# Kernel optimization log

Measured on AMD Instinct MI355X. Metric: run time of the kernel, lower is better.

The kernel has to match this reference:

```python
import jax, jax.numpy as jnp
import numpy as np

EPSILON = 1e-8
DT = 0.1
STEPS = 3
MASK_DENSITY = 0.01


def setup_inputs() -> dict:
    key = jax.random.key(0)
    k1, k2 = jax.random.split(key)
    B, S, D = 4, 4096, 2
    psi = jax.random.normal(k1, (B, S, D), dtype=jnp.float32)
    # binary mask: threshold a uniform draw to get a sparse 0/1 adjacency
    u = jax.random.uniform(k2, (B, S, S), dtype=jnp.float32)
    binary_mask = (u < MASK_DENSITY).astype(jnp.float32)
    return {"psi": psi, "binary_mask": binary_mask}


def reference(psi, binary_mask):
    def force(state):
        # adjacency-weighted aggregation minus self: [B,S,S] @ [B,S,2]
        return jnp.einsum('bij,bjd->bid', binary_mask, state) - state

    def step(p, _):
        r = jnp.linalg.norm(p, axis=-1, keepdims=True)          # [B,S,1]
        k1 = force(p)
        psi_star = p + DT * k1
        star_norm = jnp.linalg.norm(psi_star, axis=-1, keepdims=True)
        psi_star = psi_star * (r / (star_norm + EPSILON))       # renormalize to r
        k2 = force(psi_star)
        p_new = p + 0.5 * DT * (k1 + k2)
        new_norm = jnp.linalg.norm(p_new, axis=-1, keepdims=True)
        p_new = p_new * (r / (new_norm + EPSILON))              # norm-preserving
        return p_new, None

    psi_out, _ = jax.lax.scan(step, psi, None, length=STEPS)
    return psi_out
```

## Files before the change

### kernel.cpp

```cpp
#include <hip/hip_runtime.h>
#include <stdint.h>

#define BATCH   4
#define SEQ     4096
#define NROWS   (BATCH * SEQ)
#define SLOTS   80
#define SENT    SEQ
#define PSTR    4224
#define DTS     0.1f
#define HALF_DT 0.05f
#define EPS     1e-8f

typedef float fx4 __attribute__((ext_vector_type(4)));

__device__ __forceinline__ float2 ballot_force_sum(unsigned long long w,
                                                   const float2* __restrict__ gb,
                                                   int lane) {
    const int colbase = ((lane >> 2) << 8) | (lane & 3);
    float sx = 0.f, sy = 0.f;
    while (w) {
        int j = __builtin_ctzll(w);
        w &= (w - 1);
        float2 v = gb[colbase + (j << 2)];
        sx += v.x; sy += v.y;
    }
#pragma unroll
    for (int m = 32; m >= 1; m >>= 1) {
        sx += __shfl_xor(sx, m, 64);
        sy += __shfl_xor(sy, m, 64);
    }
    return make_float2(sx, sy);
}

__global__ __launch_bounds__(256)
void compress_phaseA(const float* __restrict__ mask,
                     const float2* __restrict__ psi,
                     ushort* __restrict__ idx,
                     float2* __restrict__ k1buf,
                     float2* __restrict__ star,
                     float2* __restrict__ pbuf,
                     float*  __restrict__ rbuf) {
    const int row  = (blockIdx.x * blockDim.x + threadIdx.x) >> 6;
    const int lane = threadIdx.x & 63;

    const fx4* src = reinterpret_cast<const fx4*>(mask + (size_t)row * SEQ);
    unsigned long long word = 0ull;
#pragma unroll
    for (int c = 0; c < 16; ++c) {
        fx4 v = __builtin_nontemporal_load(&src[c * 64 + lane]);
        unsigned long long b;
        b = __ballot(v.x != 0.f); if (lane == c * 4 + 0) word = b;
        b = __ballot(v.y != 0.f); if (lane == c * 4 + 1) word = b;
        b = __ballot(v.z != 0.f); if (lane == c * 4 + 2) word = b;
        b = __ballot(v.w != 0.f); if (lane == c * 4 + 3) word = b;
    }

    int pc  = __popcll(word);
    int inc = pc;
#pragma unroll
    for (int ofs = 1; ofs < 64; ofs <<= 1) {
        int t = __shfl_up(inc, ofs, 64);
        if (lane >= ofs) inc += t;
    }
    int pos   = inc - pc;
    int total = __shfl(inc, 63, 64);

    ushort* dst = idx + (size_t)row * SLOTS;
    const int colbase = ((lane >> 2) << 8) | (lane & 3);
    unsigned long long w = word;
    while (w) {
        int j = __builtin_ctzll(w);
        w &= (w - 1);
        if (pos < SLOTS) dst[pos] = (ushort)(colbase + (j << 2));
        ++pos;
    }
    for (int s = total + lane; s < SLOTS; s += 64) dst[s] = (ushort)SENT;

    const int bidx = row >> 12;
    const int rloc = row & 4095;
    float2 sum = ballot_force_sum(word, psi + ((size_t)bidx << 12), lane);
    float2 p  = psi[row];
    float r   = sqrtf(p.x * p.x + p.y * p.y);
    float k1x = sum.x - p.x, k1y = sum.y - p.y;
    float tx  = p.x + DTS * k1x, ty = p.y + DTS * k1y;
    float sc  = r / (sqrtf(tx * tx + ty * ty) + EPS);
    if (lane == 0) {
        k1buf[row] = make_float2(k1x, k1y);
        rbuf[row]  = r;
        star[(size_t)bidx * PSTR + rloc] = make_float2(tx * sc, ty * sc);
        if (rloc == 0) {
            star[(size_t)bidx * PSTR + SENT] = make_float2(0.f, 0.f);
            pbuf[(size_t)bidx * PSTR + SENT] = make_float2(0.f, 0.f);
        }
    }
}

template <int PHASE>
__global__ __launch_bounds__(256)
void force_step(const ushort* __restrict__ idx,
                const float2* __restrict__ pIn, int pinStr,
                const float2* __restrict__ gath,
                float2* __restrict__ k1buf,
                float*  __restrict__ rbuf,
                float2* __restrict__ outbuf, int outStr) {
    __shared__ float2 lds[SEQ + 2];
    const int tid  = blockIdx.x * blockDim.x + threadIdx.x;
    const int row  = tid >> 4;
    const int q    = tid & 15;
    const int bidx = row >> 12;
    const int rloc = row & 4095;
    const float2* __restrict__ gb = gath + (size_t)bidx * PSTR;

    {
        const float4* __restrict__ g4 = reinterpret_cast<const float4*>(gb);
        float4* l4 = reinterpret_cast<float4*>(lds);
#pragma unroll
        for (int t = 0; t < 8; ++t)
            l4[threadIdx.x + t * 256] = g4[threadIdx.x + t * 256];
        if (threadIdx.x == 0) lds[SENT] = gb[SENT];
    }

    const ushort* __restrict__ ip = idx + (size_t)row * SLOTS;
    int c[5];
#pragma unroll
    for (int r = 0; r < 5; ++r) c[r] = ip[q * 5 + r];
    float2 pg = make_float2(0.f, 0.f), k1 = make_float2(0.f, 0.f);
    float  rv = 0.f;
    if (PHASE == 1) {
        pg = pIn[(size_t)bidx * pinStr + rloc];
        k1 = k1buf[row];
        rv = rbuf[row];
    }

    __syncthreads();

    float sx = 0.f, sy = 0.f;
#pragma unroll
    for (int r = 0; r < 5; ++r) {
        float2 v = lds[c[r]];
        sx += v.x; sy += v.y;
    }
#pragma unroll
    for (int m = 8; m >= 1; m >>= 1) {
        sx += __shfl_xor(sx, m, 64);
        sy += __shfl_xor(sy, m, 64);
    }

    if (q == 0) {
        if (PHASE == 0) {
            float2 p  = lds[rloc];
            float r   = sqrtf(p.x * p.x + p.y * p.y);
            float k1x = sx - p.x, k1y = sy - p.y;
            float tx  = p.x + DTS * k1x, ty = p.y + DTS * k1y;
            float sc  = r / (sqrtf(tx * tx + ty * ty) + EPS);
            k1buf[row] = make_float2(k1x, k1y);
            rbuf[row]  = r;
            outbuf[(size_t)bidx * outStr + rloc] = make_float2(tx * sc, ty * sc);
        } else {
            float2 st = lds[rloc];
            float k2x = sx - st.x, k2y = sy - st.y;
            float nx  = pg.x + HALF_DT * (k1.x + k2x);
            float ny  = pg.y + HALF_DT * (k1.y + k2y);
            float sc  = rv / (sqrtf(nx * nx + ny * ny) + EPS);
            outbuf[(size_t)bidx * outStr + rloc] = make_float2(nx * sc, ny * sc);
        }
    }
}

extern "C" void kernel_launch(void* const* d_in, const int* in_sizes, int n_in,
                              void* d_out, int out_size, void* d_ws, size_t ws_size,
                              hipStream_t stream) {
    const float* psi  = (const float*)d_in[0];
    const float* mask = (const float*)d_in[1];
    float2* out2 = (float2*)d_out;

    char* ws = (char*)d_ws;
    ushort* idx = (ushort*)ws;
    float2* pbuf = (float2*)(ws + (size_t)NROWS * SLOTS * sizeof(ushort));
    float2* star = pbuf + (size_t)BATCH * PSTR;
    float2* k1   = star + (size_t)BATCH * PSTR;
    float*  rbuf = (float*)(k1 + NROWS);

    const float2* psi2 = (const float2*)psi;

    compress_phaseA<<<NROWS / 4, 256, 0, stream>>>(mask, psi2, idx, k1, star, pbuf, rbuf);
    force_step<1><<<NROWS / 16, 256, 0, stream>>>(idx, psi2, SEQ, star, k1, rbuf, pbuf, PSTR);
    force_step<0><<<NROWS / 16, 256, 0, stream>>>(idx, pbuf, PSTR, pbuf, k1, rbuf, star, PSTR);
    force_step<1><<<NROWS / 16, 256, 0, stream>>>(idx, pbuf, PSTR, star, k1, rbuf, pbuf, PSTR);
    force_step<0><<<NROWS / 16, 256, 0, stream>>>(idx, pbuf, PSTR, pbuf, k1, rbuf, star, PSTR);
    force_step<1><<<NROWS / 16, 256, 0, stream>>>(idx, pbuf, PSTR, star, k1, rbuf, out2, SEQ);
}
```

Measured before the change: 355.5 us.

## Fuse five force-step launches into one persistent kernel with grid barriers

Replaces the five separate force_step launches with a single persistent kernel of 256 blocks of 1024 threads, separated by a software grid-wide atomic barrier. The goal is to remove per-launch overhead and kernel drain/fill gaps between the small force phases. Each block now reloads its batch's source vector into LDS every phase, and the sentinel slot is zeroed in LDS instead of global memory. It relies on all 256 blocks being co-resident, risks deadlock if they are not, and adds spin-wait and memset costs.

```diff
diff --git a/kernel.cpp b/kernel.cpp
--- a/kernel.cpp
+++ b/kernel.cpp
@@ -6,10 +6,12 @@
 #define NROWS   (BATCH * SEQ)
 #define SLOTS   80
 #define SENT    SEQ
-#define PSTR    4224
 #define DTS     0.1f
 #define HALF_DT 0.05f
 #define EPS     1e-8f
+
+#define NBLK    256
+#define NTHR    1024
 
 typedef float fx4 __attribute__((ext_vector_type(4)));
 
@@ -37,8 +39,7 @@
                      const float2* __restrict__ psi,
                      ushort* __restrict__ idx,
                      float2* __restrict__ k1buf,
-                     float2* __restrict__ star,
-                     float2* __restrict__ pbuf,
+                     float2* __restrict__ starbuf,
                      float*  __restrict__ rbuf) {
     const int row  = (blockIdx.x * blockDim.x + threadIdx.x) >> 6;
     const int lane = threadIdx.x & 63;
@@ -77,7 +78,6 @@
     for (int s = total + lane; s < SLOTS; s += 64) dst[s] = (ushort)SENT;
 
     const int bidx = row >> 12;
-    const int rloc = row & 4095;
     float2 sum = ballot_force_sum(word, psi + ((size_t)bidx << 12), lane);
     float2 p  = psi[row];
     float r   = sqrtf(p.x * p.x + p.y * p.y);
@@ -85,85 +85,105 @@
     float tx  = p.x + DTS * k1x, ty = p.y + DTS * k1y;
     float sc  = r / (sqrtf(tx * tx + ty * ty) + EPS);
     if (lane == 0) {
-        k1buf[row] = make_float2(k1x, k1y);
-        rbuf[row]  = r;
-        star[(size_t)bidx * PSTR + rloc] = make_float2(tx * sc, ty * sc);
-        if (rloc == 0) {
-            star[(size_t)bidx * PSTR + SENT] = make_float2(0.f, 0.f);
-            pbuf[(size_t)bidx * PSTR + SENT] = make_float2(0.f, 0.f);
-        }
-    }
-}
-
-template <int PHASE>
-__global__ __launch_bounds__(256)
-void force_step(const ushort* __restrict__ idx,
-                const float2* __restrict__ pIn, int pinStr,
-                const float2* __restrict__ gath,
-                float2* __restrict__ k1buf,
-                float*  __restrict__ rbuf,
-                float2* __restrict__ outbuf, int outStr) {
-    __shared__ float2 lds[SEQ + 2];
-    const int tid  = blockIdx.x * blockDim.x + threadIdx.x;
-    const int row  = tid >> 4;
-    const int q    = tid & 15;
+        k1buf[row]   = make_float2(k1x, k1y);
+        rbuf[row]    = r;
+        starbuf[row] = make_float2(tx * sc, ty * sc);
+    }
+}
+
+__device__ __forceinline__ void gbar(int* __restrict__ bar, int gen) {
+    __syncthreads();
+    if (threadIdx.x == 0) {
+        __threadfence();
+        atomicAdd(bar, 1);
+        while (__hip_atomic_load(bar, __ATOMIC_RELAXED,
+                                 __HIP_MEMORY_SCOPE_AGENT) < gen * NBLK)
+            __builtin_amdgcn_s_sleep(2);
+        __threadfence();
+    }
+    __syncthreads();
+}
+
+__global__ __launch_bounds__(NTHR)
+void forces(const ushort* __restrict__ idx,
+            const float2* __restrict__ psi,
+            float2* __restrict__ pbuf,
+            float2* __restrict__ star,
+            float2* __restrict__ k1buf,
+            float*  __restrict__ rbuf,
+            float2* __restrict__ out,
+            int*    __restrict__ bar) {
+    __shared__ float2 SRC[SEQ + 2];
+
+    const int t    = threadIdx.x;
+    const int g    = t >> 4;
+    const int q    = t & 15;
+    const int row  = (blockIdx.x << 6) + g;
     const int bidx = row >> 12;
     const int rloc = row & 4095;
-    const float2* __restrict__ gb = gath + (size_t)bidx * PSTR;
-
-    {
-        const float4* __restrict__ g4 = reinterpret_cast<const float4*>(gb);
-        float4* l4 = reinterpret_cast<float4*>(lds);
-#pragma unroll
-        for (int t = 0; t < 8; ++t)
-            l4[threadIdx.x + t * 256] = g4[threadIdx.x + t * 256];
-        if (threadIdx.x == 0) lds[SENT] = gb[SENT];
-    }
+    const size_t bo = (size_t)bidx << 12;
 
     const ushort* __restrict__ ip = idx + (size_t)row * SLOTS;
     int c[5];
 #pragma unroll
     for (int r = 0; r < 5; ++r) c[r] = ip[q * 5 + r];
-    float2 pg = make_float2(0.f, 0.f), k1 = make_float2(0.f, 0.f);
-    float  rv = 0.f;
-    if (PHASE == 1) {
-        pg = pIn[(size_t)bidx * pinStr + rloc];
-        k1 = k1buf[row];
-        rv = rbuf[row];
-    }
-
-    __syncthreads();
-
-    float sx = 0.f, sy = 0.f;
-#pragma unroll
-    for (int r = 0; r < 5; ++r) {
-        float2 v = lds[c[r]];
-        sx += v.x; sy += v.y;
-    }
-#pragma unroll
-    for (int m = 8; m >= 1; m >>= 1) {
-        sx += __shfl_xor(sx, m, 64);
-        sy += __shfl_xor(sy, m, 64);
-    }
-
-    if (q == 0) {
-        if (PHASE == 0) {
-            float2 p  = lds[rloc];
-            float r   = sqrtf(p.x * p.x + p.y * p.y);
-            float k1x = sx - p.x, k1y = sy - p.y;
-            float tx  = p.x + DTS * k1x, ty = p.y + DTS * k1y;
-            float sc  = r / (sqrtf(tx * tx + ty * ty) + EPS);
-            k1buf[row] = make_float2(k1x, k1y);
-            rbuf[row]  = r;
-            outbuf[(size_t)bidx * outStr + rloc] = make_float2(tx * sc, ty * sc);
-        } else {
-            float2 st = lds[rloc];
-            float k2x = sx - st.x, k2y = sy - st.y;
-            float nx  = pg.x + HALF_DT * (k1.x + k2x);
-            float ny  = pg.y + HALF_DT * (k1.y + k2y);
-            float sc  = rv / (sqrtf(nx * nx + ny * ny) + EPS);
-            outbuf[(size_t)bidx * outStr + rloc] = make_float2(nx * sc, ny * sc);
-        }
+
+    int gen = 0;
+#pragma unroll 1
+    for (int ph = 0; ph < 5; ++ph) {
+        const bool isA = (ph & 1);
+        const float2* __restrict__ gb = (isA ? pbuf : star) + bo;
+
+        {
+            const float4* __restrict__ s4 = reinterpret_cast<const float4*>(gb);
+            float4* l4 = reinterpret_cast<float4*>(SRC);
+            l4[t] = s4[t];
+            l4[t + 1024] = s4[t + 1024];
+            if (t == 0) SRC[SEQ] = make_float2(0.f, 0.f);
+        }
+        float2 p = make_float2(0.f, 0.f), k1 = make_float2(0.f, 0.f);
+        float  rv = 0.f;
+        if (!isA) {
+            p  = (ph == 0) ? psi[row] : pbuf[row];
+            k1 = k1buf[row];
+            rv = rbuf[row];
+        }
+        __syncthreads();
+
+        float sx = 0.f, sy = 0.f;
+#pragma unroll
+        for (int r = 0; r < 5; ++r) {
+            float2 v = SRC[c[r]];
+            sx += v.x; sy += v.y;
+        }
+#pragma unroll
+        for (int m = 8; m >= 1; m >>= 1) {
+            sx += __shfl_xor(sx, m, 64);
+            sy += __shfl_xor(sy, m, 64);
+        }
+
+        if (q == 0) {
+            if (isA) {
+                float2 ps = SRC[rloc];
+                float r   = sqrtf(ps.x * ps.x + ps.y * ps.y);
+                float k1x = sx - ps.x, k1y = sy - ps.y;
+                float tx  = ps.x + DTS * k1x, ty = ps.y + DTS * k1y;
+                float sc  = r / (sqrtf(tx * tx + ty * ty) + EPS);
+                k1buf[row] = make_float2(k1x, k1y);
+                rbuf[row]  = r;
+                star[row]  = make_float2(tx * sc, ty * sc);
+            } else {
+                float2 st = SRC[rloc];
+                float k2x = sx - st.x, k2y = sy - st.y;
+                float nx  = p.x + HALF_DT * (k1.x + k2x);
+                float ny  = p.y + HALF_DT * (k1.y + k2y);
+                float sc  = rv / (sqrtf(nx * nx + ny * ny) + EPS);
+                float2 pn = make_float2(nx * sc, ny * sc);
+                if (ph == 4) out[row]  = pn;
+                else         pbuf[row] = pn;
+            }
+        }
+        if (ph < 4) gbar(bar, ++gen);
     }
 }
 
@@ -175,18 +195,16 @@
     float2* out2 = (float2*)d_out;
 
     char* ws = (char*)d_ws;
-    ushort* idx = (ushort*)ws;
+    ushort* idx  = (ushort*)ws;
     float2* pbuf = (float2*)(ws + (size_t)NROWS * SLOTS * sizeof(ushort));
-    float2* star = pbuf + (size_t)BATCH * PSTR;
-    float2* k1   = star + (size_t)BATCH * PSTR;
+    float2* star = pbuf + NROWS;
+    float2* k1   = star + NROWS;
     float*  rbuf = (float*)(k1 + NROWS);
+    int*    bar  = (int*)(rbuf + NROWS);
 
     const float2* psi2 = (const float2*)psi;
 
-    compress_phaseA<<<NROWS / 4, 256, 0, stream>>>(mask, psi2, idx, k1, star, pbuf, rbuf);
-    force_step<1><<<NROWS / 16, 256, 0, stream>>>(idx, psi2, SEQ, star, k1, rbuf, pbuf, PSTR);
-    force_step<0><<<NROWS / 16, 256, 0, stream>>>(idx, pbuf, PSTR, pbuf, k1, rbuf, star, PSTR);
-    force_step<1><<<NROWS / 16, 256, 0, stream>>>(idx, pbuf, PSTR, star, k1, rbuf, pbuf, PSTR);
-    force_step<0><<<NROWS / 16, 256, 0, stream>>>(idx, pbuf, PSTR, pbuf, k1, rbuf, star, PSTR);
-    force_step<1><<<NROWS / 16, 256, 0, stream>>>(idx, pbuf, PSTR, star, k1, rbuf, out2, SEQ);
-}
+    hipMemsetAsync(bar, 0, 64, stream);
+    compress_phaseA<<<NROWS / 4, 256, 0, stream>>>(mask, psi2, idx, k1, star, rbuf);
+    forces<<<NBLK, NTHR, 0, stream>>>(idx, psi2, pbuf, star, k1, rbuf, out2, bar);
+}
```

Result: slower. 406.9 us (+14.4%).
